# Performance work log

Measured on AMD Instinct MI355X. Metric: run time of the kernel, lower is better.

Reference implementation:

```python
import jax, jax.numpy as jnp
import numpy as np
from jax import lax

B, T, I, H = 32, 1024, 512, 1024


def setup_inputs() -> dict:
    key = jax.random.key(0)
    k1, k2, k3, k4, k5 = jax.random.split(key, 5)
    s = 1.0 / np.sqrt(H)
    return {
        "inputs": jax.random.normal(k1, (B, T, I), dtype=jnp.float32),
        "W_ih": jax.random.normal(k2, (4 * H, I), dtype=jnp.float32) * s,
        "W_hh": jax.random.normal(k3, (4 * H, H), dtype=jnp.float32) * s,
        "b_ih": jax.random.normal(k4, (4 * H,), dtype=jnp.float32) * s,
        "b_hh": jax.random.normal(k5, (4 * H,), dtype=jnp.float32) * s,
    }


def reference(inputs, W_ih, W_hh, b_ih, b_hh):
    # inputs: [B, T, I]; torch LSTMCell gate order: i, f, g, o
    b = inputs.shape[0]
    h0 = jnp.zeros((b, H), dtype=inputs.dtype)
    c0 = jnp.zeros((b, H), dtype=inputs.dtype)
    xs = jnp.transpose(inputs, (1, 0, 2))  # [T, B, I]

    def step(carry, x_t):
        h, c = carry
        gates = x_t @ W_ih.T + b_ih + h @ W_hh.T + b_hh  # [B, 4H]
        i_g, f_g, g_g, o_g = jnp.split(gates, 4, axis=-1)
        i_g = jax.nn.sigmoid(i_g)
        f_g = jax.nn.sigmoid(f_g)
        g_g = jnp.tanh(g_g)
        o_g = jax.nn.sigmoid(o_g)
        c_new = f_g * c + i_g * g_g
        h_new = o_g * jnp.tanh(c_new)
        return (h_new, c_new), h_new

    (h_T, c_T), ys = lax.scan(step, (h0, c0), xs)
    outputs = jnp.transpose(ys, (1, 0, 2))  # [B, T, H]
    return outputs, h_T, c_T
```

## Files before the change

### kernel.cpp

```cpp
#include <hip/hip_runtime.h>
#include <stdint.h>
#include <stddef.h>

#define Bn 32
#define Tn 1024
#define In 512
#define Hn 1024
#define NBLK 32
#define NTHR 256
#define GP 132

typedef _Float16 half8 __attribute__((ext_vector_type(8)));
typedef float float4x __attribute__((ext_vector_type(4)));
#define MFMA(a, b, c) __builtin_amdgcn_mfma_f32_16x16x32_f16((a), (b), (c), 0, 0, 0)


__global__ void prep_w_k(const float* __restrict__ Wih, const float* __restrict__ Whh,
                         const float* __restrict__ bih, const float* __restrict__ bhh,
                         _Float16* __restrict__ Wp, float* __restrict__ bias) {
  int nb = blockIdx.x;
  for (int p = threadIdx.x; p < 8 * 48 * 64; p += blockDim.x) {
    int nt = p / (48 * 64);
    int rem = p % (48 * 64);
    int kc = rem >> 6, lane = rem & 63;
    int row = ((nt >> 1) << 10) + (nb << 5) + ((nt & 1) << 4) + (lane & 15);
    int kb = (kc << 5) + ((lane >> 4) << 3);
    half8 v;
#pragma unroll
    for (int j = 0; j < 8; ++j) {
      int k = kb + j;
      float w = (k < In) ? Wih[(size_t)row * In + k] : Whh[(size_t)row * Hn + (k - In)];
      v[j] = (_Float16)w;
    }
    *(half8*)(Wp + (((size_t)nb * 8 + nt) * 48 + kc) * 512 + lane * 8) = v;
  }
  if (threadIdx.x < 128) {
    int nt = threadIdx.x >> 4, r = threadIdx.x & 15;
    int row = ((nt >> 1) << 10) + (nb << 5) + ((nt & 1) << 4) + r;
    bias[nb * 128 + threadIdx.x] = bih[row] + bhh[row];
  }
}

__global__ void prep_x_k(const float* __restrict__ x, _Float16* __restrict__ xp) {
  int t = blockIdx.x;
  for (int p = threadIdx.x; p < 2048; p += blockDim.x) {
    int mt = p >> 10, rem = p & 1023, kc = rem >> 6, lane = rem & 63;
    int b = (lane & 15) + (mt << 4);
    int k = (kc << 5) + ((lane >> 4) << 3);
    const float* src = x + ((size_t)b * Tn + t) * In + k;
    half8 v;
#pragma unroll
    for (int j = 0; j < 8; ++j) v[j] = (_Float16)src[j];
    *(half8*)(xp + ((size_t)(t * 2 + mt) * 16 + kc) * 512 + lane * 8) = v;
  }
}

__global__ __launch_bounds__(NTHR, 1) void lstm_k(
    const _Float16* __restrict__ xp, const _Float16* __restrict__ Wp,
    const float* __restrict__ bias, _Float16* __restrict__ hp,
    int* __restrict__ flags, float* __restrict__ out) {
  __shared__ __attribute__((aligned(16))) _Float16 hs[2 * 32 * 512];
  __shared__ float gbuf[32 * GP];

  const int tid = threadIdx.x;
  const int wave = tid >> 6, lane = tid & 63;
  const int nb = blockIdx.x;
  const int nt0 = wave, nt1 = wave + 4;
  const int g0 = nt0 >> 1, h0_ = nt0 & 1;
  const int g1 = nt1 >> 1, h1_ = nt1 & 1;

  half8 wx0[16], wx1[16], wh0[32], wh1[32];
  {
    const _Float16* b0 = Wp + ((size_t)nb * 8 + nt0) * 48 * 512;
    const _Float16* b1 = Wp + ((size_t)nb * 8 + nt1) * 48 * 512;
#pragma unroll
    for (int kc = 0; kc < 16; ++kc) {
      wx0[kc] = *(const half8*)(b0 + (size_t)kc * 512 + lane * 8);
      wx1[kc] = *(const half8*)(b1 + (size_t)kc * 512 + lane * 8);
    }
#pragma unroll
    for (int kc = 0; kc < 32; ++kc) {
      wh0[kc] = *(const half8*)(b0 + (size_t)(16 + kc) * 512 + lane * 8);
      wh1[kc] = *(const half8*)(b1 + (size_t)(16 + kc) * 512 + lane * 8);
    }
  }
#pragma unroll
  for (int i = 0; i < 16; ++i) {
    asm volatile("" : "+v"(wx0[i]));
    asm volatile("" : "+v"(wx1[i]));
  }
#pragma unroll
  for (int i = 0; i < 32; ++i) {
    asm volatile("" : "+v"(wh0[i]));
    asm volatile("" : "+v"(wh1[i]));
  }
  const float bv0 = bias[nb * 128 + nt0 * 16 + (lane & 15)];
  const float bv1 = bias[nb * 128 + nt1 * 16 + (lane & 15)];

  const int pb = tid >> 3, pc = tid & 7;
  float cr[4] = {0.f, 0.f, 0.f, 0.f};

  float4x a00 = {0.f, 0.f, 0.f, 0.f}, a01 = {0.f, 0.f, 0.f, 0.f};
  float4x a10 = {0.f, 0.f, 0.f, 0.f}, a11 = {0.f, 0.f, 0.f, 0.f};
  {
    const _Float16* xb = xp;
#pragma unroll
    for (int kc = 0; kc < 16; ++kc) {
      half8 x0 = *(const half8*)(xb + (size_t)kc * 512 + lane * 8);
      half8 x1 = *(const half8*)(xb + (size_t)(16 + kc) * 512 + lane * 8);
      a00 = MFMA(x0, wx0[kc], a00);
      a01 = MFMA(x0, wx1[kc], a01);
      a10 = MFMA(x1, wx0[kc], a10);
      a11 = MFMA(x1, wx1[kc], a11);
    }
  }

  for (int t = 0; t < Tn; ++t) {
    const int cur = t & 1;

    {
      const unsigned long long* hsrc =
          (const unsigned long long*)(hp + (size_t)cur * 32768);
      unsigned long long tmp[32];
#pragma unroll
      for (int i = 0; i < 32; ++i)
        tmp[i] = __hip_atomic_load(hsrc + tid + i * 256,
                                   __ATOMIC_RELAXED, __HIP_MEMORY_SCOPE_AGENT);
      unsigned long long* hdst = (unsigned long long*)hs;
#pragma unroll
      for (int i = 0; i < 32; ++i) hdst[tid + i * 256] = tmp[i];
    }
    __syncthreads();

#pragma unroll
    for (int kc = 0; kc < 32; ++kc) {
      half8 ha0 = *(const half8*)(hs + (size_t)kc * 512 + lane * 8);
      half8 ha1 = *(const half8*)(hs + (size_t)(32 + kc) * 512 + lane * 8);
      a00 = MFMA(ha0, wh0[kc], a00);
      a01 = MFMA(ha0, wh1[kc], a01);
      a10 = MFMA(ha1, wh0[kc], a10);
      a11 = MFMA(ha1, wh1[kc], a11);
    }

    {
      const int r0 = (lane >> 4) * 4;
      const int c0 = g0 * 32 + h0_ * 16 + (lane & 15);
      const int c1 = g1 * 32 + h1_ * 16 + (lane & 15);
#pragma unroll
      for (int r = 0; r < 4; ++r) {
        gbuf[(r0 + r) * GP + c0] = a00[r] + bv0;
        gbuf[(r0 + r) * GP + c1] = a01[r] + bv1;
        gbuf[(16 + r0 + r) * GP + c0] = a10[r] + bv0;
        gbuf[(16 + r0 + r) * GP + c1] = a11[r] + bv1;
      }
    }
    __syncthreads();

    {
      const int col = pc * 4;
      const float* gr = gbuf + pb * GP;
      float hv[4];
#pragma unroll
      for (int c = 0; c < 4; ++c) {
        float gi = gr[col + c], gf = gr[32 + col + c];
        float gg = gr[64 + col + c], go = gr[96 + col + c];
        float i_ = 1.f / (1.f + __expf(-gi));
        float f_ = 1.f / (1.f + __expf(-gf));
        float g_ = 1.f - 2.f / (1.f + __expf(2.f * gg));
        float o_ = 1.f / (1.f + __expf(-go));
        cr[c] = f_ * cr[c] + i_ * g_;
        hv[c] = o_ * (1.f - 2.f / (1.f + __expf(2.f * cr[c])));
      }

      size_t ob = ((size_t)pb * Tn + t) * Hn + nb * 32 + col;
      float4x ov = {hv[0], hv[1], hv[2], hv[3]};
      *(float4x*)(out + ob) = ov;

      union { _Float16 h[4]; unsigned long long u; } pk;
#pragma unroll
      for (int c = 0; c < 4; ++c) pk.h[c] = (_Float16)hv[c];
      const int mtp = pb >> 4;
      const int lanep = (pb & 15) + (((col >> 3) & 3) << 4);
      size_t hoff = ((size_t)((cur ^ 1) * 2 + mtp) * 32 + nb) * 512 + lanep * 8 + (col & 7);
      __hip_atomic_store((unsigned long long*)(hp + hoff), pk.u,
                         __ATOMIC_RELAXED, __HIP_MEMORY_SCOPE_AGENT);

      if (t == Tn - 1) {
        size_t base = (size_t)Bn * Tn * Hn;
        float4x cv = {cr[0], cr[1], cr[2], cr[3]};
        *(float4x*)(out + base + (size_t)pb * Hn + nb * 32 + col) = ov;
        *(float4x*)(out + base + (size_t)Bn * Hn + (size_t)pb * Hn + nb * 32 + col) = cv;
      }
    }

    __syncthreads();

    if (tid == 0)
      __hip_atomic_store(flags + nb * 16, t + 1, __ATOMIC_RELAXED, __HIP_MEMORY_SCOPE_AGENT);

    {
      a00 = (float4x){0.f, 0.f, 0.f, 0.f};
      a01 = (float4x){0.f, 0.f, 0.f, 0.f};
      a10 = (float4x){0.f, 0.f, 0.f, 0.f};
      a11 = (float4x){0.f, 0.f, 0.f, 0.f};
      const int tn = (t + 1 < Tn) ? t + 1 : t;
      const _Float16* xb = xp + (size_t)tn * 2 * 16 * 512;
#pragma unroll
      for (int kc = 0; kc < 16; ++kc) {
        half8 x0 = *(const half8*)(xb + (size_t)kc * 512 + lane * 8);
        half8 x1 = *(const half8*)(xb + (size_t)(16 + kc) * 512 + lane * 8);
        a00 = MFMA(x0, wx0[kc], a00);
        a01 = MFMA(x0, wx1[kc], a01);
        a10 = MFMA(x1, wx0[kc], a10);
        a11 = MFMA(x1, wx1[kc], a11);
      }
    }

    if (wave == 0) {
      const int tgt = t + 1;
      for (;;) {
        int v = tgt;
        if (lane < NBLK)
          v = __hip_atomic_load(flags + lane * 16, __ATOMIC_RELAXED, __HIP_MEMORY_SCOPE_AGENT);
        if (__all(v >= tgt)) break;
        __builtin_amdgcn_s_sleep(1);
      }
    }
    __syncthreads();
  }
}

extern "C" void kernel_launch(void* const* d_in, const int* in_sizes, int n_in,
                              void* d_out, int out_size, void* d_ws, size_t ws_size,
                              hipStream_t stream) {
  const float* x   = (const float*)d_in[0];
  const float* Wih = (const float*)d_in[1];
  const float* Whh = (const float*)d_in[2];
  const float* bih = (const float*)d_in[3];
  const float* bhh = (const float*)d_in[4];
  float* out = (float*)d_out;

  char* ws = (char*)d_ws;
  _Float16* Wp   = (_Float16*)ws;
  float*    bias = (float*)(ws + (size_t)6291456 * 2);
  _Float16* xp   = (_Float16*)(ws + (size_t)6291456 * 2 + 16384);
  _Float16* hp   = xp + (size_t)16777216;
  int*      flags = (int*)(hp + 65536);

  prep_w_k<<<NBLK, 256, 0, stream>>>(Wih, Whh, bih, bhh, Wp, bias);
  prep_x_k<<<Tn, 256, 0, stream>>>(x, xp);
  hipMemsetAsync(hp, 0, 32768 * sizeof(_Float16), stream);
  hipMemsetAsync(flags, 0, NBLK * 16 * sizeof(int), stream);
  lstm_k<<<NBLK, NTHR, 0, stream>>>(xp, Wp, bias, hp, flags, out);
}
```

Before: 12.03 ms.

## Pin persistent LSTM blocks to one XCC and use sc0 cache-coherent loads

Launches 256 blocks, reads each block's XCC id and elects the first XCC to collect 32 blocks; only those blocks run the recurrence and the rest exit. Keeping all workers on one XCC lets the h exchange and the flag barrier go through that XCC's shared L2 instead of device-scope coherence. The atomics are also replaced by inline-asm global loads and stores with sc0, plus explicit waitcnts. This relies on the hardware scheduler placing at least 32 blocks on some XCC and on the undocumented coherence behaviour of sc0. Bounded spin loops are added as well.

```diff
diff --git a/kernel.cpp b/kernel.cpp
--- a/kernel.cpp
+++ b/kernel.cpp
@@ -7,6 +7,7 @@
 #define In 512
 #define Hn 1024
 #define NBLK 32
+#define NGRID 256
 #define NTHR 256
 #define GP 132
 
@@ -61,10 +62,33 @@
     int* __restrict__ flags, float* __restrict__ out) {
   __shared__ __attribute__((aligned(16))) _Float16 hs[2 * 32 * 512];
   __shared__ float gbuf[32 * GP];
+  __shared__ int s_slot;
 
   const int tid = threadIdx.x;
   const int wave = tid >> 6, lane = tid & 63;
-  const int nb = blockIdx.x;
+
+  {
+    unsigned xcc;
+    asm volatile("s_getreg_b32 %0, hwreg(HW_REG_XCC_ID)" : "=s"(xcc));
+    xcc &= 7;
+    if (tid == 0) {
+      int* ctr = flags + 512;
+      int* elect = flags + 520;
+      int slot = atomicAdd(&ctr[xcc], 1);
+      if (slot == NBLK - 1) atomicCAS(elect, 0, (int)xcc + 1);
+      int e = 0;
+      for (long i = 0; i < 200000000L; ++i) {
+        e = __hip_atomic_load(elect, __ATOMIC_RELAXED, __HIP_MEMORY_SCOPE_AGENT);
+        if (e != 0) break;
+        __builtin_amdgcn_s_sleep(8);
+      }
+      s_slot = (e == (int)xcc + 1 && slot < NBLK) ? slot : -1;
+    }
+  }
+  __syncthreads();
+  const int nb = s_slot;
+  if (nb < 0) return;
+
   const int nt0 = wave, nt1 = wave + 4;
   const int g0 = nt0 >> 1, h0_ = nt0 & 1;
   const int g1 = nt1 >> 1, h1_ = nt1 & 1;
@@ -119,13 +143,15 @@
     const int cur = t & 1;
 
     {
-      const unsigned long long* hsrc =
-          (const unsigned long long*)(hp + (size_t)cur * 32768);
+      const uint64_t sbase = (uint64_t)(hp + (size_t)cur * 32768);
+      const unsigned voff0 = (unsigned)(tid * 8);
       unsigned long long tmp[32];
 #pragma unroll
       for (int i = 0; i < 32; ++i)
-        tmp[i] = __hip_atomic_load(hsrc + tid + i * 256,
-                                   __ATOMIC_RELAXED, __HIP_MEMORY_SCOPE_AGENT);
+        asm volatile("global_load_dwordx2 %0, %1, %2 sc0"
+                     : "=&v"(tmp[i]) : "v"(voff0 + i * 2048u), "s"(sbase));
+      asm volatile("s_waitcnt vmcnt(0)" ::: "memory");
+      __builtin_amdgcn_sched_barrier(0);
       unsigned long long* hdst = (unsigned long long*)hs;
 #pragma unroll
       for (int i = 0; i < 32; ++i) hdst[tid + i * 256] = tmp[i];
@@ -182,8 +208,8 @@
       const int mtp = pb >> 4;
       const int lanep = (pb & 15) + (((col >> 3) & 3) << 4);
       size_t hoff = ((size_t)((cur ^ 1) * 2 + mtp) * 32 + nb) * 512 + lanep * 8 + (col & 7);
-      __hip_atomic_store((unsigned long long*)(hp + hoff), pk.u,
-                         __ATOMIC_RELAXED, __HIP_MEMORY_SCOPE_AGENT);
+      asm volatile("global_store_dwordx2 %0, %1, off sc0"
+                   :: "v"((uint64_t)(hp + hoff)), "v"(pk.u) : "memory");
 
       if (t == Tn - 1) {
         size_t base = (size_t)Bn * Tn * Hn;
@@ -193,10 +219,12 @@
       }
     }
 
+    asm volatile("s_waitcnt vmcnt(0)" ::: "memory");
     __syncthreads();
 
     if (tid == 0)
-      __hip_atomic_store(flags + nb * 16, t + 1, __ATOMIC_RELAXED, __HIP_MEMORY_SCOPE_AGENT);
+      asm volatile("global_store_dword %0, %1, off sc0"
+                   :: "v"((uint64_t)(flags + nb * 16)), "v"(t + 1) : "memory");
 
     {
       a00 = (float4x){0.f, 0.f, 0.f, 0.f};
@@ -218,10 +246,11 @@
 
     if (wave == 0) {
       const int tgt = t + 1;
-      for (;;) {
-        int v = tgt;
-        if (lane < NBLK)
-          v = __hip_atomic_load(flags + lane * 16, __ATOMIC_RELAXED, __HIP_MEMORY_SCOPE_AGENT);
+      const uint64_t pa = (uint64_t)(flags + (lane & (NBLK - 1)) * 16);
+      for (int it = 0; it < 30000000; ++it) {
+        int v;
+        asm volatile("global_load_dword %0, %1, off sc0\n\ts_waitcnt vmcnt(0)"
+                     : "=v"(v) : "v"(pa) : "memory");
         if (__all(v >= tgt)) break;
         __builtin_amdgcn_s_sleep(1);
       }
@@ -250,6 +279,6 @@
   prep_w_k<<<NBLK, 256, 0, stream>>>(Wih, Whh, bih, bhh, Wp, bias);
   prep_x_k<<<Tn, 256, 0, stream>>>(x, xp);
   hipMemsetAsync(hp, 0, 32768 * sizeof(_Float16), stream);
-  hipMemsetAsync(flags, 0, NBLK * 16 * sizeof(int), stream);
-  lstm_k<<<NBLK, NTHR, 0, stream>>>(xp, Wp, bias, hp, flags, out);
-}
+  hipMemsetAsync(flags, 0, (512 + 16) * sizeof(int), stream);
+  lstm_k<<<NGRID, NTHR, 0, stream>>>(xp, Wp, bias, hp, flags, out);
+}
```

Measured after the change: 12.12 ms. About the same (+0.8%).
